# Performance work log

Hardware: AMD Instinct MI355X
Metric: run time of the kernel (lower is better)

## Reference

```python
import jax, jax.numpy as jnp
import numpy as np

B, C, H, W = 8, 256, 64, 64


def conv1x1(x, w, b):
    # x: (n,c,h,w), w: (o,c), b: (o,)
    return jnp.einsum('oc,nchw->nohw', w, x) + b[None, :, None, None]


def maxpool2(x):
    return jax.lax.reduce_window(x, -jnp.inf, jax.lax.max,
                                 (1, 1, 2, 2), (1, 1, 2, 2), 'VALID')


def setup_inputs() -> dict:
    key = jax.random.key(0)
    ks = jax.random.split(key, 10)
    d = C // 8   # 32
    dv = C // 2  # 128
    s = 0.05
    return {
        'x': jax.random.normal(ks[0], (B, C, H, W), jnp.float32),
        'theta_w': jax.random.normal(ks[1], (d, C), jnp.float32) * s,
        'theta_b': jax.random.normal(ks[2], (d,), jnp.float32) * s,
        'phi_w': jax.random.normal(ks[3], (d, C), jnp.float32) * s,
        'phi_b': jax.random.normal(ks[4], (d,), jnp.float32) * s,
        'g_w': jax.random.normal(ks[5], (dv, C), jnp.float32) * s,
        'g_b': jax.random.normal(ks[6], (dv,), jnp.float32) * s,
        'out_w': jax.random.normal(ks[7], (C, dv), jnp.float32) * s,
        'out_b': jax.random.normal(ks[8], (C,), jnp.float32) * s,
        'gamma': jnp.array([0.3], jnp.float32),  # nn.Parameter scalar (init 0 in torch; nonzero here for nontrivial output)
    }


def reference(x, theta_w, theta_b, phi_w, phi_b, g_w, g_b, out_w, out_b, gamma):
    n, c, h, w = x.shape
    N, M = h * w, (h // 2) * (w // 2)
    # queries: (n, N, d)
    theta = conv1x1(x, theta_w, theta_b).reshape(n, c // 8, N).transpose(0, 2, 1)
    # keys (pooled): (n, d, M)
    phi = maxpool2(conv1x1(x, phi_w, phi_b)).reshape(n, c // 8, M)
    energy = jnp.einsum('nid,ndj->nij', theta, phi)          # (n, N, M)
    attention = jax.nn.softmax(energy, axis=-1)
    # values (pooled): (n, dv, M)
    g = maxpool2(conv1x1(x, g_w, g_b)).reshape(n, c // 2, M)
    out = jnp.einsum('ncj,nij->nci', g, attention)           # (n, dv, N)
    out = out.reshape(n, c // 2, h, w)
    out = conv1x1(out, out_w, out_b)
    return gamma * out + x
```

## Files before the change

### kernel.cpp

```cpp
#include <hip/hip_runtime.h>
#include <hip/hip_bf16.h>
#include <cstddef>

typedef __attribute__((ext_vector_type(8))) short short8;
typedef __attribute__((ext_vector_type(4))) float f32x4;
typedef __attribute__((ext_vector_type(4))) unsigned int u32x4;
typedef __attribute__((ext_vector_type(2))) unsigned int u32x2;

__device__ __forceinline__ unsigned short f2bf(float f) {
    union { float f; unsigned int u; } v; v.f = f;
    unsigned int r = v.u + 0x7fffu + ((v.u >> 16) & 1u);
    return (unsigned short)(r >> 16);
}
__device__ __forceinline__ unsigned int pack2bf(float lo, float hi) {
    __hip_bfloat162 h2 = __float22bfloat162_rn(make_float2(lo, hi));
    union { __hip_bfloat162 h; unsigned int u; } v; v.h = h2;
    return v.u;
}

__global__ __launch_bounds__(256) void cvt_k(const float* __restrict__ tw,
    const float* __restrict__ tb, const float* __restrict__ pw, const float* __restrict__ pb,
    const float* __restrict__ gw, const float* __restrict__ gb, const float* __restrict__ ow,
    unsigned short* __restrict__ wb, unsigned short* __restrict__ owb, float* __restrict__ bcat)
{
    int idx = blockIdx.x * 256 + threadIdx.x;
    if (idx < 49152) {
        int o = idx >> 8, c = idx & 255;
        float v = (o < 32) ? tw[o * 256 + c] : (o < 64) ? pw[(o - 32) * 256 + c]
                                             : gw[(o - 64) * 256 + c];
        wb[idx] = f2bf(v);
    } else if (idx < 81920) {
        owb[idx - 49152] = f2bf(ow[idx - 49152]);
    } else if (idx < 82112) {
        int o = idx - 81920;
        bcat[o] = (o < 32) ? tb[o] : (o < 64) ? pb[o - 32] : gb[o - 64];
    }
}

__global__ __launch_bounds__(256) void conv_qkv_k(const float* __restrict__ x,
    const unsigned short* __restrict__ wb, const float* __restrict__ bcat,
    unsigned short* __restrict__ theta, unsigned short* __restrict__ phi_f,
    unsigned short* __restrict__ g_f)
{
    __shared__ __align__(16) unsigned int xT[2][32 * 24];
    int bx = blockIdx.x;
    int n  = blockIdx.y;
    int rp = bx >> 2, cq = bx & 3;
    int t = threadIdx.x;
    int w = t >> 6;
    int l = t & 63;
    int lg = l >> 4, ll = l & 15;

    int p = t & 31, co = t >> 5;
    int gpix_s = (2 * rp + (p >> 4)) * 64 + cq * 16 + (p & 15);
    const float* xp = x + (size_t)n * 256 * 4096 + gpix_s;

    const f32x4 zero = {0.f, 0.f, 0.f, 0.f};
    f32x4 acc[3][2];
    #pragma unroll
    for (int mt = 0; mt < 3; ++mt)
        #pragma unroll
        for (int nt = 0; nt < 2; ++nt) acc[mt][nt] = zero;

    {
        float xv[4];
        #pragma unroll
        for (int u = 0; u < 4; ++u) xv[u] = xp[(size_t)(co * 4 + u) * 4096];
        u32x2 pk = {pack2bf(xv[0], xv[1]), pack2bf(xv[2], xv[3])};
        *(u32x2*)&xT[0][p * 24 + co * 2] = pk;
    }
    for (int kk = 0; kk < 8; ++kk) {
        __syncthreads();
        float nv[4];
        if (kk < 7) {
            #pragma unroll
            for (int u = 0; u < 4; ++u)
                nv[u] = xp[(size_t)((kk + 1) * 32 + co * 4 + u) * 4096];
        }
        int ko = kk * 32 + lg * 8;
        short8 af[3];
        #pragma unroll
        for (int mt = 0; mt < 3; ++mt)
            af[mt] = *(const short8*)(wb + (size_t)(w * 48 + mt * 16 + ll) * 256 + ko);
        #pragma unroll
        for (int nt = 0; nt < 2; ++nt) {
            short8 bf = *(const short8*)&xT[kk & 1][(nt * 16 + ll) * 24 + lg * 4];
            #pragma unroll
            for (int mt = 0; mt < 3; ++mt)
                acc[mt][nt] = __builtin_amdgcn_mfma_f32_16x16x32_bf16(af[mt], bf, acc[mt][nt], 0, 0, 0);
        }
        if (kk < 7) {
            u32x2 pk = {pack2bf(nv[0], nv[1]), pack2bf(nv[2], nv[3])};
            *(u32x2*)&xT[(kk + 1) & 1][p * 24 + co * 2] = pk;
        }
    }

    int jj = cq * 8 + (ll >> 1);
    #pragma unroll
    for (int mt = 0; mt < 3; ++mt) {
        int obase = w * 48 + mt * 16;
        if (obase < 32) {
            #pragma unroll
            for (int nt = 0; nt < 2; ++nt) {
                int gpix = (2 * rp + nt) * 64 + cq * 16 + ll;
                float v0 = acc[mt][nt][0] + bcat[obase + lg * 4 + 0];
                float v1 = acc[mt][nt][1] + bcat[obase + lg * 4 + 1];
                float v2 = acc[mt][nt][2] + bcat[obase + lg * 4 + 2];
                float v3 = acc[mt][nt][3] + bcat[obase + lg * 4 + 3];
                u32x2 pk = {pack2bf(v0, v1), pack2bf(v2, v3)};
                *(u32x2*)&theta[((size_t)(n * 4096 + gpix)) * 32 + obase + lg * 4] = pk;
            }
        } else if (obase < 64) {
            int d0 = obase - 32;
            float vv[4];
            #pragma unroll
            for (int r = 0; r < 4; ++r) {
                float v = fmaxf(acc[mt][0][r], acc[mt][1][r]);
                vv[r] = fmaxf(v, __shfl_xor(v, 1)) + bcat[obase + lg * 4 + r];
            }
            if (!(ll & 1)) {
                int s = (jj >> 2) & 1;
                int llp = ((jj >> 3) << 2) | (jj & 3);
                int lgp = (d0 >> 3) + (lg >> 1);
                size_t idx = ((((size_t)n * 32 + rp) * 2 + s) * 64 + lgp * 16 + llp) * 8
                           + (lg & 1) * 4;
                u32x2 pk = {pack2bf(vv[0], vv[1]), pack2bf(vv[2], vv[3])};
                *(u32x2*)&phi_f[idx] = pk;
            }
        } else {
            int ct = (obase - 64) >> 4;
            float vv[4];
            #pragma unroll
            for (int r = 0; r < 4; ++r) {
                float v = fmaxf(acc[mt][0][r], acc[mt][1][r]);
                vv[r] = fmaxf(v, __shfl_xor(v, 1)) + bcat[obase + lg * 4 + r];
            }
            if (!(ll & 1)) {
                int lgg = jj >> 3, uu = jj & 7;
                size_t base = ((((size_t)n * 32 + rp) * 8 + ct) * 64 + lgg * 16) * 8 + uu;
                #pragma unroll
                for (int r = 0; r < 4; ++r)
                    g_f[base + (size_t)(lg * 4 + r) * 8] = f2bf(vv[r]);
            }
        }
    }
}

__global__ __launch_bounds__(256, 4) void attn_k(const unsigned short* __restrict__ theta,
    const unsigned short* __restrict__ phi_f, const unsigned short* __restrict__ g_f,
    unsigned short* __restrict__ att_p)
{
    __shared__ float comb[2][64][34];
    int b = blockIdx.x;
    int swz = (b & 7) * 128 + (b >> 3);
    int n = swz >> 7;
    int i0 = (swz & 127) * 32;
    int t = threadIdx.x;
    int wv = t >> 6;
    int h = wv >> 1, v = wv & 1;
    int l = t & 63;
    int lg = l >> 4, ll = l & 15;
    int i0w = i0 + h * 16;

    short8 bfrag = *(const short8*)(theta + ((size_t)(n * 4096 + i0w + ll)) * 32 + lg * 8);
    const unsigned short* phin = phi_f + (size_t)n * 32768;
    const unsigned short* gfn  = g_f + (size_t)n * 131072;

    const f32x4 zero = {0.f, 0.f, 0.f, 0.f};
    f32x4 acc[8];
    #pragma unroll
    for (int ct = 0; ct < 8; ++ct) acc[ct] = zero;
    float rs = 0.f;

    #pragma unroll 2
    for (int jt = 0; jt < 16; ++jt) {
        int jtg = v * 16 + jt;
        short8 a0 = *(const short8*)(phin + (size_t)jtg * 1024 + l * 8);
        short8 a1 = *(const short8*)(phin + (size_t)jtg * 1024 + 512 + l * 8);
        f32x4 e0 = __builtin_amdgcn_mfma_f32_16x16x32_bf16(a0, bfrag, zero, 0, 0, 0);
        f32x4 e1 = __builtin_amdgcn_mfma_f32_16x16x32_bf16(a1, bfrag, zero, 0, 0, 0);
        float p0[4], p1[4];
        #pragma unroll
        for (int r = 0; r < 4; ++r) {
            p0[r] = __expf(e0[r]); p1[r] = __expf(e1[r]);
            rs += p0[r] + p1[r];
        }
        union { u32x4 u; short8 s; } cv;
        cv.u = (u32x4){pack2bf(p0[0], p0[1]), pack2bf(p0[2], p0[3]),
                       pack2bf(p1[0], p1[1]), pack2bf(p1[2], p1[3])};
        short8 pa = cv.s;
        const unsigned short* gj = gfn + (size_t)jtg * 4096 + l * 8;
        #pragma unroll
        for (int ct = 0; ct < 8; ++ct) {
            short8 gb = *(const short8*)(gj + ct * 512);
            acc[ct] = __builtin_amdgcn_mfma_f32_16x16x32_bf16(pa, gb, acc[ct], 0, 0, 0);
        }
    }

    rs += __shfl_xor(rs, 16);
    rs += __shfl_xor(rs, 32);

    if (v == 1) {
        #pragma unroll
        for (int ct = 0; ct < 8; ++ct)
            #pragma unroll
            for (int r = 0; r < 4; ++r)
                comb[h][l][ct * 4 + r] = acc[ct][r];
        if (lg == 0) comb[h][ll][32] = rs;
    }
    __syncthreads();
    if (v == 0) {
        float inv = 1.f / (rs + comb[h][ll][32]);
        float invr[4];
        #pragma unroll
        for (int r = 0; r < 4; ++r) invr[r] = __shfl(inv, lg * 4 + r);
        #pragma unroll
        for (int ct = 0; ct < 8; ++ct) {
            int c = ct * 16 + ll;
            #pragma unroll
            for (int r = 0; r < 4; ++r) {
                float val = acc[ct][r] + comb[h][l][ct * 4 + r];
                att_p[((size_t)(n * 4096 + i0w + lg * 4 + r)) * 128 + c]
                    = f2bf(val * invr[r]);
            }
        }
    }
}

__global__ __launch_bounds__(256) void out_mfma_k(const unsigned short* __restrict__ att_p,
    const unsigned short* __restrict__ owb, const float* __restrict__ ob,
    const float* __restrict__ x, const float* __restrict__ gamma, float* __restrict__ out)
{
    int px0 = blockIdx.x * 32;
    int n  = blockIdx.y;
    int t = threadIdx.x;
    int w = t >> 6;
    int l = t & 63;
    int lg = l >> 4, ll = l & 15;

    const unsigned short* abase = att_p + ((size_t)(n * 4096 + px0)) * 128;
    const f32x4 zero = {0.f, 0.f, 0.f, 0.f};
    f32x4 acc[4][2];
    #pragma unroll
    for (int mt = 0; mt < 4; ++mt)
        #pragma unroll
        for (int nt = 0; nt < 2; ++nt) acc[mt][nt] = zero;

    #pragma unroll
    for (int kk = 0; kk < 4; ++kk) {
        int ko = kk * 32 + lg * 8;
        short8 af[4];
        #pragma unroll
        for (int mt = 0; mt < 4; ++mt)
            af[mt] = *(const short8*)(owb + (size_t)(w * 64 + mt * 16 + ll) * 128 + ko);
        #pragma unroll
        for (int nt = 0; nt < 2; ++nt) {
            short8 bf = *(const short8*)(abase + (size_t)(nt * 16 + ll) * 128 + ko);
            #pragma unroll
            for (int mt = 0; mt < 4; ++mt)
                acc[mt][nt] = __builtin_amdgcn_mfma_f32_16x16x32_bf16(af[mt], bf, acc[mt][nt], 0, 0, 0);
        }
    }

    float gm = gamma[0];
    #pragma unroll
    for (int mt = 0; mt < 4; ++mt)
        #pragma unroll
        for (int nt = 0; nt < 2; ++nt)
            #pragma unroll
            for (int r = 0; r < 4; ++r) {
                int o = w * 64 + mt * 16 + lg * 4 + r;
                size_t oi = ((size_t)(n * 256 + o)) * 4096 + px0 + nt * 16 + ll;
                out[oi] = fmaf(gm, acc[mt][nt][r] + ob[o], x[oi]);
            }
}

extern "C" void kernel_launch(void* const* d_in, const int* in_sizes, int n_in,
                              void* d_out, int out_size, void* d_ws, size_t ws_size,
                              hipStream_t stream) {
    const float* x       = (const float*)d_in[0];
    const float* theta_w = (const float*)d_in[1];
    const float* theta_b = (const float*)d_in[2];
    const float* phi_w   = (const float*)d_in[3];
    const float* phi_b   = (const float*)d_in[4];
    const float* g_w     = (const float*)d_in[5];
    const float* g_b     = (const float*)d_in[6];
    const float* out_w   = (const float*)d_in[7];
    const float* out_b   = (const float*)d_in[8];
    const float* gamma   = (const float*)d_in[9];
    float* out = (float*)d_out;

    char* w8 = (char*)d_ws;
    unsigned short* wb    = (unsigned short*)(w8);
    unsigned short* owb   = (unsigned short*)(w8 + 98304);
    float*          bcat  = (float*)         (w8 + 163840);
    unsigned short* theta = (unsigned short*)(w8 + 164864);
    unsigned short* phi_f = (unsigned short*)(w8 + 2262016);
    unsigned short* g_f   = (unsigned short*)(w8 + 2786304);
    unsigned short* att_p = (unsigned short*)(w8 + 4883456);

    cvt_k<<<321, 256, 0, stream>>>(theta_w, theta_b, phi_w, phi_b, g_w, g_b, out_w,
                                   wb, owb, bcat);
    conv_qkv_k<<<dim3(128, 8), 256, 0, stream>>>(x, wb, bcat, theta, phi_f, g_f);
    attn_k<<<1024, 256, 0, stream>>>(theta, phi_f, g_f, att_p);
    out_mfma_k<<<dim3(128, 8), 256, 0, stream>>>(att_p, owb, out_b, x, gamma, out);
}
```

Before: 153.6 us.

## Fuse attention and output 1x1 conv into one kernel via LDS staging

The attention kernel now writes its normalized bf16 output tile into shared memory instead of a global att_p buffer, then performs the output 1x1 conv MFMA, bias, gamma scaling and residual add in the same block. The out_w weights are pre-permuted into MFMA fragment order so each lane loads a contiguous short8. This removes one kernel launch and the global write/read round trip of the attention output. In exchange it adds extra LDS (about 8.7KB) and a barrier to a kernel pinned at 4 blocks per SM, which may reduce occupancy or raise register pressure.

```diff
diff --git a/kernel.cpp b/kernel.cpp
--- a/kernel.cpp
+++ b/kernel.cpp
@@ -21,7 +21,7 @@
 __global__ __launch_bounds__(256) void cvt_k(const float* __restrict__ tw,
     const float* __restrict__ tb, const float* __restrict__ pw, const float* __restrict__ pb,
     const float* __restrict__ gw, const float* __restrict__ gb, const float* __restrict__ ow,
-    unsigned short* __restrict__ wb, unsigned short* __restrict__ owb, float* __restrict__ bcat)
+    unsigned short* __restrict__ wb, unsigned short* __restrict__ owf, float* __restrict__ bcat)
 {
     int idx = blockIdx.x * 256 + threadIdx.x;
     if (idx < 49152) {
@@ -30,7 +30,12 @@
                                              : gw[(o - 64) * 256 + c];
         wb[idx] = f2bf(v);
     } else if (idx < 81920) {
-        owb[idx - 49152] = f2bf(ow[idx - 49152]);
+        int i2 = idx - 49152;
+        int o = i2 >> 7, c = i2 & 127;
+        int w = o >> 6, mt = (o >> 4) & 3, llp = o & 15;
+        int kk = c >> 5, lg = (c >> 3) & 3, u = c & 7;
+        size_t pos = ((((size_t)(w * 4 + mt) * 4 + kk) * 64) + lg * 16 + llp) * 8 + u;
+        owf[pos] = f2bf(ow[i2]);
     } else if (idx < 82112) {
         int o = idx - 81920;
         bcat[o] = (o < 32) ? tb[o] : (o < 64) ? pb[o - 32] : gb[o - 64];
@@ -146,11 +151,13 @@
     }
 }
 
-__global__ __launch_bounds__(256, 4) void attn_k(const unsigned short* __restrict__ theta,
+__global__ __launch_bounds__(256, 4) void attn_out_k(const unsigned short* __restrict__ theta,
     const unsigned short* __restrict__ phi_f, const unsigned short* __restrict__ g_f,
-    unsigned short* __restrict__ att_p)
+    const unsigned short* __restrict__ owf, const float* __restrict__ ob,
+    const float* __restrict__ x, const float* __restrict__ gamma, float* __restrict__ out)
 {
     __shared__ float comb[2][64][34];
+    __shared__ __align__(16) unsigned short att_lds[32][136];
     int b = blockIdx.x;
     int swz = (b & 7) * 128 + (b >> 3);
     int n = swz >> 7;
@@ -220,45 +227,31 @@
             #pragma unroll
             for (int r = 0; r < 4; ++r) {
                 float val = acc[ct][r] + comb[h][l][ct * 4 + r];
-                att_p[((size_t)(n * 4096 + i0w + lg * 4 + r)) * 128 + c]
-                    = f2bf(val * invr[r]);
-            }
-        }
-    }
-}
-
-__global__ __launch_bounds__(256) void out_mfma_k(const unsigned short* __restrict__ att_p,
-    const unsigned short* __restrict__ owb, const float* __restrict__ ob,
-    const float* __restrict__ x, const float* __restrict__ gamma, float* __restrict__ out)
-{
-    int px0 = blockIdx.x * 32;
-    int n  = blockIdx.y;
-    int t = threadIdx.x;
-    int w = t >> 6;
-    int l = t & 63;
-    int lg = l >> 4, ll = l & 15;
-
-    const unsigned short* abase = att_p + ((size_t)(n * 4096 + px0)) * 128;
-    const f32x4 zero = {0.f, 0.f, 0.f, 0.f};
-    f32x4 acc[4][2];
+                att_lds[h * 16 + lg * 4 + r][c] = f2bf(val * invr[r]);
+            }
+        }
+    }
+    __syncthreads();
+
+    f32x4 acc2[4][2];
     #pragma unroll
     for (int mt = 0; mt < 4; ++mt)
         #pragma unroll
-        for (int nt = 0; nt < 2; ++nt) acc[mt][nt] = zero;
+        for (int nt = 0; nt < 2; ++nt) acc2[mt][nt] = zero;
 
     #pragma unroll
     for (int kk = 0; kk < 4; ++kk) {
-        int ko = kk * 32 + lg * 8;
         short8 af[4];
         #pragma unroll
         for (int mt = 0; mt < 4; ++mt)
-            af[mt] = *(const short8*)(owb + (size_t)(w * 64 + mt * 16 + ll) * 128 + ko);
+            af[mt] = *(const short8*)(owf
+                + ((((size_t)(wv * 4 + mt) * 4 + kk) * 64) + l) * 8);
         #pragma unroll
         for (int nt = 0; nt < 2; ++nt) {
-            short8 bf = *(const short8*)(abase + (size_t)(nt * 16 + ll) * 128 + ko);
+            short8 bf = *(const short8*)&att_lds[nt * 16 + ll][kk * 32 + lg * 8];
             #pragma unroll
             for (int mt = 0; mt < 4; ++mt)
-                acc[mt][nt] = __builtin_amdgcn_mfma_f32_16x16x32_bf16(af[mt], bf, acc[mt][nt], 0, 0, 0);
+                acc2[mt][nt] = __builtin_amdgcn_mfma_f32_16x16x32_bf16(af[mt], bf, acc2[mt][nt], 0, 0, 0);
         }
     }
 
@@ -269,9 +262,9 @@
         for (int nt = 0; nt < 2; ++nt)
             #pragma unroll
             for (int r = 0; r < 4; ++r) {
-                int o = w * 64 + mt * 16 + lg * 4 + r;
-                size_t oi = ((size_t)(n * 256 + o)) * 4096 + px0 + nt * 16 + ll;
-                out[oi] = fmaf(gm, acc[mt][nt][r] + ob[o], x[oi]);
+                int o = wv * 64 + mt * 16 + lg * 4 + r;
+                size_t oi = ((size_t)(n * 256 + o)) * 4096 + i0 + nt * 16 + ll;
+                out[oi] = fmaf(gm, acc2[mt][nt][r] + ob[o], x[oi]);
             }
 }
 
@@ -292,16 +285,14 @@
 
     char* w8 = (char*)d_ws;
     unsigned short* wb    = (unsigned short*)(w8);
-    unsigned short* owb   = (unsigned short*)(w8 + 98304);
+    unsigned short* owf   = (unsigned short*)(w8 + 98304);
     float*          bcat  = (float*)         (w8 + 163840);
     unsigned short* theta = (unsigned short*)(w8 + 164864);
     unsigned short* phi_f = (unsigned short*)(w8 + 2262016);
     unsigned short* g_f   = (unsigned short*)(w8 + 2786304);
-    unsigned short* att_p = (unsigned short*)(w8 + 4883456);
 
     cvt_k<<<321, 256, 0, stream>>>(theta_w, theta_b, phi_w, phi_b, g_w, g_b, out_w,
-                                   wb, owb, bcat);
+                                   wb, owf, bcat);
     conv_qkv_k<<<dim3(128, 8), 256, 0, stream>>>(x, wb, bcat, theta, phi_f, g_f);
-    attn_k<<<1024, 256, 0, stream>>>(theta, phi_f, g_f, att_p);
-    out_mfma_k<<<dim3(128, 8), 256, 0, stream>>>(att_p, owb, out_b, x, gamma, out);
-}
+    attn_out_k<<<1024, 256, 0, stream>>>(theta, phi_f, g_f, owf, out_b, x, gamma, out);
+}
```

After: 139.1 us. -9.4%, faster.
